# Kernel tuning notes

Hardware: AMD Instinct MI355X
Metric: run time of the kernel (lower is better)

The kernel has to match this reference:

```python
import jax, jax.numpy as jnp
import numpy as np


def setup_inputs() -> dict:
    key = jax.random.key(0)
    ks = jax.random.split(key, 5)
    B, N, D = 8, 2048, 512
    return {
        "query": jax.random.normal(ks[0], (B, N, D), dtype=jnp.float32),
        "key": jax.random.normal(ks[1], (B, N, D), dtype=jnp.float32),
        "value": jax.random.normal(ks[2], (B, N, D), dtype=jnp.float32),
        "w_k": jax.random.normal(ks[3], (2 * N - 1, D), dtype=jnp.float32),
        "w_v": jax.random.normal(ks[4], (2 * N - 1, D), dtype=jnp.float32),
    }


def reference(query, key, value, w_k, w_v):
    B, N, D = query.shape
    # skew indices: idx[i, j] = (N-1) - i + j  maps (i,j) -> relative distance j-i,
    # distance 0 sits at the middle column (N-1) of the 2N-1 relative table.
    idx = (N - 1) - jnp.arange(N)[:, None] + jnp.arange(N)[None, :]  # [N, N]

    # content scores: [B, N, N]
    base_scores = jnp.einsum("bqd,bkd->bqk", query, key)
    # relative key scores: matmul against full 2N-1 table then skewed gather
    all_rel = jnp.einsum("bqd,rd->bqr", query, w_k)  # [B, N, 2N-1]
    rel_scores = jnp.take_along_axis(
        all_rel, jnp.broadcast_to(idx[None], (B, N, N)), axis=-1
    )
    p_attn = jax.nn.softmax(base_scores + rel_scores, axis=-1)  # [B, N, N]

    # value path: scatter probabilities into skewed [B, N, 2N-1] layout,
    # then one matmul against the relative value table (equivalent to
    # sum_j p[i,j] * w_v[(N-1)-i+j]).
    rows = jnp.arange(N)[:, None]  # [N, 1] broadcast against idx [N, N]
    p_skew = jnp.zeros((B, N, 2 * N - 1), dtype=p_attn.dtype)
    p_skew = p_skew.at[:, rows, idx].set(p_attn)
    rel_out = jnp.einsum("bqr,rd->bqd", p_skew, w_v)

    out = jnp.einsum("bqk,bkd->bqd", p_attn, value) + rel_out
    return out, p_attn
```

## Files before the change

kernel.cpp:

```cpp
#include <hip/hip_runtime.h>


#define SEQN 2048
#define DD   512
#define NB   8
#define WROWS 4095
#define WPAD  4096

typedef float     f32x4 __attribute__((ext_vector_type(4)));
typedef _Float16  h16x4 __attribute__((ext_vector_type(4)));
typedef _Float16  h16x8 __attribute__((ext_vector_type(8)));

__device__ __forceinline__ unsigned swzw(int row, int c4) {
  unsigned b = (unsigned)(row * 64 + c4 * 8);
  return b ^ (((unsigned)row & 6u) << 3);
}
__device__ __forceinline__ unsigned swzr(int row, int kg) {
  unsigned b = (unsigned)(row * 64 + kg * 16);
  return b ^ (((unsigned)row & 6u) << 3);
}

__global__ __launch_bounds__(256) void transpose_v_k(const float* __restrict__ v,
                                                     _Float16* __restrict__ vT) {
  __shared__ float tile[32][33];
  const int d0 = blockIdx.x * 32, j0 = blockIdx.y * 32, b = blockIdx.z;
  const int tid = threadIdx.x;
#pragma unroll
  for (int rep = 0; rep < 4; rep++) {
    int idx = rep * 256 + tid;
    int rr = idx >> 5, cc = idx & 31;
    tile[rr][cc] = v[((size_t)(b * SEQN + j0 + rr)) * DD + d0 + cc];
  }
  __syncthreads();
#pragma unroll
  for (int rep = 0; rep < 4; rep++) {
    int idx = rep * 256 + tid;
    int rr = idx >> 5, cc = idx & 31;
    vT[((size_t)(b * DD + d0 + rr)) * SEQN + j0 + cc] = (_Float16)tile[cc][rr];
  }
}

__global__ __launch_bounds__(256) void transpose_wv_k(const float* __restrict__ wv,
                                                      _Float16* __restrict__ wvT) {
  __shared__ float tile[32][33];
  const int d0 = blockIdx.x * 32, r0 = blockIdx.y * 32;
  const int tid = threadIdx.x;
#pragma unroll
  for (int rep = 0; rep < 4; rep++) {
    int idx = rep * 256 + tid;
    int rr = idx >> 5, cc = idx & 31;
    float val = 0.f;
    if (r0 + rr < WROWS) val = wv[(size_t)(r0 + rr) * DD + d0 + cc];
    tile[rr][cc] = val;
  }
  __syncthreads();
#pragma unroll
  for (int rep = 0; rep < 4; rep++) {
    int idx = rep * 256 + tid;
    int rr = idx >> 5, cc = idx & 31;
    wvT[(size_t)(d0 + rr) * WPAD + r0 + cc] = (_Float16)tile[cc][rr];
  }
}

__global__ __launch_bounds__(256) void score_base4_k(const float* __restrict__ q,
                                                     const float* __restrict__ kmat,
                                                     float* __restrict__ S) {
  __shared__ __align__(16) char smem[32768];
  const int j0 = blockIdx.x * 128, i0 = blockIdx.y * 128, b = blockIdx.z;
  const int tid = threadIdx.x, lane = tid & 63, wave = tid >> 6;
  const int wm = wave >> 1, wn = wave & 1, r16 = lane & 15, kg = lane >> 4;

  const float* qb = q + (size_t)(b * SEQN + i0) * DD;
  const float* kb = kmat + (size_t)(b * SEQN + j0) * DD;

  f32x4 acc[4][4];
#pragma unroll
  for (int mf = 0; mf < 4; mf++)
#pragma unroll
    for (int nf = 0; nf < 4; nf++) acc[mf][nf] = (f32x4){0.f, 0.f, 0.f, 0.f};

  f32x4 ra[4], rb[4];
  auto LOADREGS = [&](int t) {
    const int k0 = t * 32;
#pragma unroll
    for (int rep = 0; rep < 4; rep++) {
      int f = rep * 256 + tid, row = f >> 3, c4 = f & 7;
      ra[rep] = *(const f32x4*)(qb + (size_t)row * DD + k0 + c4 * 4);
      rb[rep] = *(const f32x4*)(kb + (size_t)row * DD + k0 + c4 * 4);
    }
  };
  auto WRITE = [&](char* lb) {
#pragma unroll
    for (int rep = 0; rep < 4; rep++) {
      int f = rep * 256 + tid, row = f >> 3, c4 = f & 7;
      h16x4 ha = {(_Float16)ra[rep][0], (_Float16)ra[rep][1],
                  (_Float16)ra[rep][2], (_Float16)ra[rep][3]};
      h16x4 hb = {(_Float16)rb[rep][0], (_Float16)rb[rep][1],
                  (_Float16)rb[rep][2], (_Float16)rb[rep][3]};
      *(h16x4*)(lb + swzw(row, c4)) = ha;
      *(h16x4*)(lb + 8192 + swzw(row, c4)) = hb;
    }
  };

  LOADREGS(0);
  WRITE(smem);
  LOADREGS(1);
  __syncthreads();

  for (int t = 0; t < 16; t++) {
    char* lb = smem + (t & 1) * 16384;
    if (t + 1 < 16) WRITE(smem + ((t + 1) & 1) * 16384);
    h16x8 af[4], bf[4];
#pragma unroll
    for (int mf = 0; mf < 4; mf++)
      af[mf] = *(const h16x8*)(lb + swzr(wm * 64 + mf * 16 + r16, kg));
#pragma unroll
    for (int nf = 0; nf < 4; nf++)
      bf[nf] = *(const h16x8*)(lb + 8192 + swzr(wn * 64 + nf * 16 + r16, kg));
    if (t + 2 < 16) LOADREGS(t + 2);
#pragma unroll
    for (int mf = 0; mf < 4; mf++)
#pragma unroll
      for (int nf = 0; nf < 4; nf++)
        acc[mf][nf] = __builtin_amdgcn_mfma_f32_16x16x32_f16(af[mf], bf[nf], acc[mf][nf], 0, 0, 0);
    __syncthreads();
  }

#pragma unroll
  for (int mf = 0; mf < 4; mf++)
#pragma unroll
    for (int nf = 0; nf < 4; nf++)
#pragma unroll
      for (int r = 0; r < 4; r++) {
        int ii = wm * 64 + mf * 16 + kg * 4 + r;
        int jj = wn * 64 + nf * 16 + r16;
        S[(size_t)(b * SEQN + i0 + ii) * SEQN + j0 + jj] = acc[mf][nf][r];
      }
}

__global__ __launch_bounds__(256) void score_rel4_k(const float* __restrict__ q,
                                                    const float* __restrict__ wk,
                                                    float* __restrict__ S) {
  __shared__ __align__(16) char smem[32768];
  const int z = blockIdx.x;
  const int i0 = blockIdx.y * 128, b = blockIdx.z;
  const int tid = threadIdx.x, lane = tid & 63, wave = tid >> 6;
  const int wm = wave >> 1, wn = wave & 1, r16 = lane & 15, kg = lane >> 4;
  const int tmin = SEQN - 128 - i0;

  const float* qb = q + (size_t)(b * SEQN + i0) * DD;
  const int tb = tmin + z * 128;

  f32x4 acc[4][4];
#pragma unroll
  for (int mf = 0; mf < 4; mf++)
#pragma unroll
    for (int nf = 0; nf < 4; nf++) acc[mf][nf] = (f32x4){0.f, 0.f, 0.f, 0.f};

  f32x4 ra[4], rb[4];
  auto LOADREGS = [&](int t) {
    const int k0 = t * 32;
#pragma unroll
    for (int rep = 0; rep < 4; rep++) {
      int f = rep * 256 + tid, row = f >> 3, c4 = f & 7;
      ra[rep] = *(const f32x4*)(qb + (size_t)row * DD + k0 + c4 * 4);
      int tr = tb + row;
      if (tr > WROWS - 1) tr = WROWS - 1;
      rb[rep] = *(const f32x4*)(wk + (size_t)tr * DD + k0 + c4 * 4);
    }
  };
  auto WRITE = [&](char* lb) {
#pragma unroll
    for (int rep = 0; rep < 4; rep++) {
      int f = rep * 256 + tid, row = f >> 3, c4 = f & 7;
      h16x4 ha = {(_Float16)ra[rep][0], (_Float16)ra[rep][1],
                  (_Float16)ra[rep][2], (_Float16)ra[rep][3]};
      h16x4 hb = {(_Float16)rb[rep][0], (_Float16)rb[rep][1],
                  (_Float16)rb[rep][2], (_Float16)rb[rep][3]};
      *(h16x4*)(lb + swzw(row, c4)) = ha;
      *(h16x4*)(lb + 8192 + swzw(row, c4)) = hb;
    }
  };

  LOADREGS(0);
  WRITE(smem);
  LOADREGS(1);
  __syncthreads();

  for (int t = 0; t < 16; t++) {
    char* lb = smem + (t & 1) * 16384;
    if (t + 1 < 16) WRITE(smem + ((t + 1) & 1) * 16384);
    h16x8 af[4], bf[4];
#pragma unroll
    for (int mf = 0; mf < 4; mf++)
      af[mf] = *(const h16x8*)(lb + swzr(wm * 64 + mf * 16 + r16, kg));
#pragma unroll
    for (int nf = 0; nf < 4; nf++)
      bf[nf] = *(const h16x8*)(lb + 8192 + swzr(wn * 64 + nf * 16 + r16, kg));
    if (t + 2 < 16) LOADREGS(t + 2);
#pragma unroll
    for (int mf = 0; mf < 4; mf++)
#pragma unroll
      for (int nf = 0; nf < 4; nf++)
        acc[mf][nf] = __builtin_amdgcn_mfma_f32_16x16x32_f16(af[mf], bf[nf], acc[mf][nf], 0, 0, 0);
    __syncthreads();
  }

#pragma unroll
  for (int mf = 0; mf < 4; mf++)
#pragma unroll
    for (int nf = 0; nf < 4; nf++) {
      int bcg = z * 128 + wn * 64 + nf * 16 + r16;
#pragma unroll
      for (int r = 0; r < 4; r++) {
        int ii = wm * 64 + mf * 16 + kg * 4 + r;
        int j = bcg + ii - 127;
        if (bcg <= 2174 && j >= 0 && j < SEQN) {
          S[(size_t)(b * SEQN + i0 + ii) * SEQN + j] += acc[mf][nf][r];
        }
      }
    }
}

__global__ __launch_bounds__(256) void softmax_rows_k(float* __restrict__ S) {
  const int wid = threadIdx.x >> 6, lane = threadIdx.x & 63;
  const size_t row = (size_t)blockIdx.x * 4 + wid;
  float* p = S + row * SEQN;
  f32x4 x[8];
  float m = -3.4e38f;
#pragma unroll
  for (int c = 0; c < 8; c++) {
    x[c] = *(const f32x4*)(p + c * 256 + lane * 4);
    m = fmaxf(m, fmaxf(fmaxf(x[c][0], x[c][1]), fmaxf(x[c][2], x[c][3])));
  }
#pragma unroll
  for (int off = 32; off > 0; off >>= 1) m = fmaxf(m, __shfl_xor(m, off));
  float s = 0.f;
#pragma unroll
  for (int c = 0; c < 8; c++)
#pragma unroll
    for (int e = 0; e < 4; e++) {
      x[c][e] = __expf(x[c][e] - m);
      s += x[c][e];
    }
#pragma unroll
  for (int off = 32; off > 0; off >>= 1) s += __shfl_xor(s, off);
  float inv = 1.f / s;
#pragma unroll
  for (int c = 0; c < 8; c++) {
    x[c][0] *= inv; x[c][1] *= inv; x[c][2] *= inv; x[c][3] *= inv;
    *(f32x4*)(p + c * 256 + lane * 4) = x[c];
  }
}

__global__ __launch_bounds__(256) void out_gemm3_k(const float* __restrict__ S,
                                                   const _Float16* __restrict__ vT,
                                                   const _Float16* __restrict__ wvT,
                                                   float* __restrict__ outp) {
  __shared__ __align__(16) char smem[32768];
  const int bid = blockIdx.x;
  const int xcd = bid & 7, rr = bid >> 3;
  const int x = rr & 3, s8 = rr >> 2;
  const int sidx = xcd + 8 * s8;
  const int d0 = x * 128, i0 = (sidx & 15) * 128, b = sidx >> 4;
  const int tid = threadIdx.x, lane = tid & 63, wave = tid >> 6;
  const int wm = wave >> 1, wn = wave & 1, r16 = lane & 15, kg = lane >> 4;
  const int tmin = SEQN - 128 - i0;

  const float*    pb = S  + (size_t)(b * SEQN + i0) * SEQN;
  const _Float16* vb = vT + (size_t)(b * DD + d0) * SEQN;
  const _Float16* wb = wvT + (size_t)d0 * WPAD + tmin;

  f32x4 acc[4][4];
#pragma unroll
  for (int mf = 0; mf < 4; mf++)
#pragma unroll
    for (int nf = 0; nf < 4; nf++) acc[mf][nf] = (f32x4){0.f, 0.f, 0.f, 0.f};

  f32x4 ra[4];
  h16x4 rbv[4];

  auto LOADREGS = [&](int t) {
    if (t < 64) {
      const int k0 = t * 32;
#pragma unroll
      for (int rep = 0; rep < 4; rep++) {
        int f = rep * 256 + tid, row = f >> 3, c4 = f & 7;
        ra[rep]  = *(const f32x4*)(pb + (size_t)row * SEQN + k0 + c4 * 4);
        rbv[rep] = *(const h16x4*)(vb + (size_t)row * SEQN + k0 + c4 * 4);
      }
    } else {
      const int k0 = (t - 64) * 32;
#pragma unroll
      for (int rep = 0; rep < 4; rep++) {
        int f = rep * 256 + tid, row = f >> 3, c4 = f & 7;
        int jb = k0 + c4 * 4 + row - 127;
        const float* pr = pb + (size_t)row * SEQN;
        f32x4 v4;
#pragma unroll
        for (int e = 0; e < 4; e++) {
          int j = jb + e;
          v4[e] = (j >= 0 && j < SEQN) ? pr[j] : 0.f;
        }
        ra[rep]  = v4;
        rbv[rep] = *(const h16x4*)(wb + (size_t)row * WPAD + k0 + c4 * 4);
      }
    }
  };
  auto WRITE = [&](char* lb) {
#pragma unroll
    for (int rep = 0; rep < 4; rep++) {
      int f = rep * 256 + tid, row = f >> 3, c4 = f & 7;
      h16x4 ha = {(_Float16)ra[rep][0], (_Float16)ra[rep][1],
                  (_Float16)ra[rep][2], (_Float16)ra[rep][3]};
      *(h16x4*)(lb + swzw(row, c4)) = ha;
      *(h16x4*)(lb + 8192 + swzw(row, c4)) = rbv[rep];
    }
  };

  LOADREGS(0);
  WRITE(smem);
  LOADREGS(1);
  __syncthreads();

  for (int t = 0; t < 132; t++) {
    char* lb = smem + (t & 1) * 16384;
    if (t + 1 < 132) WRITE(smem + ((t + 1) & 1) * 16384);
    h16x8 af[4], bf[4];
#pragma unroll
    for (int mf = 0; mf < 4; mf++)
      af[mf] = *(const h16x8*)(lb + swzr(wm * 64 + mf * 16 + r16, kg));
#pragma unroll
    for (int nf = 0; nf < 4; nf++)
      bf[nf] = *(const h16x8*)(lb + 8192 + swzr(wn * 64 + nf * 16 + r16, kg));
    if (t + 2 < 132) LOADREGS(t + 2);
#pragma unroll
    for (int mf = 0; mf < 4; mf++)
#pragma unroll
      for (int nf = 0; nf < 4; nf++)
        acc[mf][nf] = __builtin_amdgcn_mfma_f32_16x16x32_f16(af[mf], bf[nf], acc[mf][nf], 0, 0, 0);
    __syncthreads();
  }

#pragma unroll
  for (int mf = 0; mf < 4; mf++)
#pragma unroll
    for (int nf = 0; nf < 4; nf++)
#pragma unroll
      for (int r = 0; r < 4; r++) {
        int ii = wm * 64 + mf * 16 + kg * 4 + r;
        int dd = wn * 64 + nf * 16 + r16;
        outp[(size_t)(b * SEQN + i0 + ii) * DD + d0 + dd] = acc[mf][nf][r];
      }
}

extern "C" void kernel_launch(void* const* d_in, const int* in_sizes, int n_in,
                              void* d_out, int out_size, void* d_ws, size_t ws_size,
                              hipStream_t stream) {
  const float* q  = (const float*)d_in[0];
  const float* k  = (const float*)d_in[1];
  const float* v  = (const float*)d_in[2];
  const float* wk = (const float*)d_in[3];
  const float* wv = (const float*)d_in[4];

  float* outp = (float*)d_out;
  float* S    = outp + (size_t)NB * SEQN * DD;

  _Float16* vT  = (_Float16*)d_ws;
  _Float16* wvT = vT + (size_t)NB * DD * SEQN;

  transpose_v_k <<<dim3(DD / 32, SEQN / 32, NB), 256, 0, stream>>>(v, vT);
  transpose_wv_k<<<dim3(DD / 32, 128),           256, 0, stream>>>(wv, wvT);
  score_base4_k <<<dim3(SEQN / 128, SEQN / 128, NB), 256, 0, stream>>>(q, k, S);
  score_rel4_k  <<<dim3(17, SEQN / 128, NB),     256, 0, stream>>>(q, wk, S);
  softmax_rows_k<<<dim3(NB * SEQN / 4),          256, 0, stream>>>(S);
  out_gemm3_k   <<<dim3(512),                    256, 0, stream>>>(S, vT, wvT, outp);
}
```

Baseline: 471.8 us.

## Split output GEMM along K into two partial-sum passes plus a reduction kernel

The fused output GEMM (probabilities times V plus the skewed relative-value part) is split along the reduction dimension into two halves: one block set covers the content part (64 k-tiles), the other the relative part (68 k-tiles). This doubles the grid from 512 to 1024 blocks so the MI355X's many CUs are better filled. Partial results go to a workspace buffer and a new elementwise kernel adds them. In exchange it adds an extra kernel launch and writes and rereads two full fp32 output-sized buffers.

```diff
diff --git a/kernel.cpp b/kernel.cpp
--- a/kernel.cpp
+++ b/kernel.cpp
@@ -253,13 +253,15 @@
   }
 }
 
-__global__ __launch_bounds__(256) void out_gemm3_k(const float* __restrict__ S,
+__global__ __launch_bounds__(256) void out_split_k(const float* __restrict__ S,
                                                    const _Float16* __restrict__ vT,
                                                    const _Float16* __restrict__ wvT,
-                                                   float* __restrict__ outp) {
+                                                   float* __restrict__ pbuf) {
   __shared__ __align__(16) char smem[32768];
   const int bid = blockIdx.x;
-  const int xcd = bid & 7, rr = bid >> 3;
+  const int part = bid >> 9;
+  const int r9 = bid & 511;
+  const int xcd = r9 & 7, rr = r9 >> 3;
   const int x = rr & 3, s8 = rr >> 2;
   const int sidx = xcd + 8 * s8;
   const int d0 = x * 128, i0 = (sidx & 15) * 128, b = sidx >> 4;
@@ -271,6 +273,9 @@
   const _Float16* vb = vT + (size_t)(b * DD + d0) * SEQN;
   const _Float16* wb = wvT + (size_t)d0 * WPAD + tmin;
 
+  const int t0 = part ? 64 : 0;
+  const int nt = part ? 68 : 64;
+
   f32x4 acc[4][4];
 #pragma unroll
   for (int mf = 0; mf < 4; mf++)
@@ -318,14 +323,14 @@
     }
   };
 
-  LOADREGS(0);
+  LOADREGS(t0);
   WRITE(smem);
-  LOADREGS(1);
-  __syncthreads();
-
-  for (int t = 0; t < 132; t++) {
-    char* lb = smem + (t & 1) * 16384;
-    if (t + 1 < 132) WRITE(smem + ((t + 1) & 1) * 16384);
+  LOADREGS(t0 + 1);
+  __syncthreads();
+
+  for (int tt = 0; tt < nt; tt++) {
+    char* lb = smem + (tt & 1) * 16384;
+    if (tt + 1 < nt) WRITE(smem + ((tt + 1) & 1) * 16384);
     h16x8 af[4], bf[4];
 #pragma unroll
     for (int mf = 0; mf < 4; mf++)
@@ -333,7 +338,7 @@
 #pragma unroll
     for (int nf = 0; nf < 4; nf++)
       bf[nf] = *(const h16x8*)(lb + 8192 + swzr(wn * 64 + nf * 16 + r16, kg));
-    if (t + 2 < 132) LOADREGS(t + 2);
+    if (tt + 2 < nt) LOADREGS(t0 + tt + 2);
 #pragma unroll
     for (int mf = 0; mf < 4; mf++)
 #pragma unroll
@@ -342,6 +347,7 @@
     __syncthreads();
   }
 
+  float* dst = pbuf + (size_t)part * NB * SEQN * DD;
 #pragma unroll
   for (int mf = 0; mf < 4; mf++)
 #pragma unroll
@@ -350,8 +356,19 @@
       for (int r = 0; r < 4; r++) {
         int ii = wm * 64 + mf * 16 + kg * 4 + r;
         int dd = wn * 64 + nf * 16 + r16;
-        outp[(size_t)(b * SEQN + i0 + ii) * DD + d0 + dd] = acc[mf][nf][r];
-      }
+        dst[(size_t)(b * SEQN + i0 + ii) * DD + d0 + dd] = acc[mf][nf][r];
+      }
+}
+
+__global__ __launch_bounds__(256) void out_add_k(const float* __restrict__ pbuf,
+                                                 float* __restrict__ outp) {
+  const long n4 = (long)NB * SEQN * DD / 4;
+  const float* p1 = pbuf + (size_t)NB * SEQN * DD;
+  for (long i = (long)blockIdx.x * 256 + threadIdx.x; i < n4; i += (long)gridDim.x * 256) {
+    f32x4 a = ((const f32x4*)pbuf)[i];
+    f32x4 b = ((const f32x4*)p1)[i];
+    ((f32x4*)outp)[i] = a + b;
+  }
 }
 
 extern "C" void kernel_launch(void* const* d_in, const int* in_sizes, int n_in,
@@ -368,11 +385,13 @@
 
   _Float16* vT  = (_Float16*)d_ws;
   _Float16* wvT = vT + (size_t)NB * DD * SEQN;
+  float*    pbuf = (float*)(wvT + (size_t)DD * WPAD);
 
   transpose_v_k <<<dim3(DD / 32, SEQN / 32, NB), 256, 0, stream>>>(v, vT);
   transpose_wv_k<<<dim3(DD / 32, 128),           256, 0, stream>>>(wv, wvT);
   score_base4_k <<<dim3(SEQN / 128, SEQN / 128, NB), 256, 0, stream>>>(q, k, S);
   score_rel4_k  <<<dim3(17, SEQN / 128, NB),     256, 0, stream>>>(q, wk, S);
   softmax_rows_k<<<dim3(NB * SEQN / 4),          256, 0, stream>>>(S);
-  out_gemm3_k   <<<dim3(512),                    256, 0, stream>>>(S, vT, wvT, outp);
-}
+  out_split_k   <<<dim3(1024),                   256, 0, stream>>>(S, vT, wvT, pbuf);
+  out_add_k     <<<dim3(2048),                   256, 0, stream>>>(pbuf, outp);
+}
```

Measured after the change: 492.4 us. 4.4% more time.
